# Optimization experiments

Measured on AMD Instinct MI355X. Metric: run time of the kernel, lower is better.

## Reference

```python
import jax, jax.numpy as jnp
import numpy as np

B, T, C, L = 256, 256, 1024, 64
NEG = jnp.float32(-1e30)  # finite stand-in for -inf (safe under exp)
EPS = 1e-7  # keras.backend.epsilon()


def setup_inputs() -> dict:
    key = jax.random.key(0)
    k1, k2 = jax.random.split(key)
    # y_pred: softmax-like probabilities (Keras ctc_batch_cost expects probs)
    y_pred = jax.random.uniform(k1, (B, T, C), dtype=jnp.float32)
    y_true = jax.random.randint(k2, (B, L), 0, C - 1, dtype=jnp.int64)  # blank = C-1 excluded
    return {"y_true": y_true, "y_pred": y_pred}


def reference(y_true, y_pred):
    # Faithful to keras.backend.ctc_batch_cost with input_length=T, label_length=L:
    # logits = log(y_pred + eps); tf.nn.ctc_loss applies log_softmax internally; blank = C-1.
    b, t, c = y_pred.shape
    l = y_true.shape[1]
    blank = c - 1
    logp = jax.nn.log_softmax(jnp.log(y_pred + EPS), axis=-1)  # [B,T,C]

    # Extended label sequence: blank, l1, blank, l2, ..., blank  (length S = 2L+1)
    s = 2 * l + 1
    ext = jnp.full((b, s), blank, dtype=y_true.dtype).at[:, 1::2].set(y_true)  # [B,S]
    pos = jnp.arange(s)
    prev2 = jnp.concatenate([jnp.full((b, 2), blank, dtype=ext.dtype), ext[:, :-2]], axis=1)
    # transition s-2 -> s allowed only for non-blank labels differing from label two back
    skip_ok = (ext != blank) & (ext != prev2) & (pos >= 2)  # [B,S]

    # Emission log-probs gathered at extended labels: [B,T,S]
    emit = jnp.take_along_axis(logp, jnp.broadcast_to(ext[:, None, :], (b, t, s)), axis=2)

    # Forward DP (log-space) over time via scan
    alpha0 = jnp.where(pos < 2, emit[:, 0, :], NEG)  # only states 0,1 reachable at t=0

    def step(alpha, emit_t):
        a1 = alpha
        a2 = jnp.concatenate([jnp.full((b, 1), NEG), alpha[:, :-1]], axis=1)
        a3 = jnp.where(skip_ok, jnp.concatenate([jnp.full((b, 2), NEG), alpha[:, :-2]], axis=1), NEG)
        m = jnp.maximum(a1, jnp.maximum(a2, a3))
        alpha_new = m + jnp.log(jnp.exp(a1 - m) + jnp.exp(a2 - m) + jnp.exp(a3 - m)) + emit_t
        return alpha_new, None

    alphaT, _ = jax.lax.scan(step, alpha0, jnp.swapaxes(emit, 0, 1)[1:])  # scan over T-1 steps

    tail = alphaT[:, s - 2:]  # valid end states: last label or final blank
    m = jnp.max(tail, axis=1)
    loglik = m + jnp.log(jnp.sum(jnp.exp(tail - m[:, None]), axis=1))
    return -loglik[:, None]  # [B,1], matches ctc_batch_cost output shape
```

## Files before the change

### kernel.cpp

```cpp
#include <hip/hip_runtime.h>
#include <hip/hip_bf16.h>


#define NEGF (-1e30f)

__device__ __forceinline__ float lse2(float a, float b) {
    float m = fmaxf(a, b);
    return m + log2f(exp2f(a - m) + exp2f(b - m));
}
__device__ __forceinline__ float lse3(float a, float b, float c) {
    float m = fmaxf(fmaxf(a, b), c);
    return m + log2f(exp2f(a - m) + exp2f(b - m) + exp2f(c - m));
}

__global__ void __launch_bounds__(1024) ctc_fused_kernel(
    const float* __restrict__ y, const int* __restrict__ lab,
    float* __restrict__ out)
{
    __shared__ float lpl_s[256][64];
    __shared__ float lpb_s[256];

    const int b    = blockIdx.x;
    const int wave = threadIdx.x >> 6;
    const int lane = threadIdx.x & 63;

    const int myLab = lab[(b << 6) + lane];

    for (int i = 0; i < 16; ++i) {
        const int t = (wave << 4) + i;
        const float* __restrict__ yr = y + ((size_t)(b * 256 + t) << 10);
        const float4* __restrict__ yr4 = (const float4*)yr;
        float4 v0 = yr4[lane];
        float4 v1 = yr4[lane + 64];
        float4 v2 = yr4[lane + 128];
        float4 v3 = yr4[lane + 192];
        float s = (v0.x + v0.y + v0.z + v0.w) + (v1.x + v1.y + v1.z + v1.w)
                + (v2.x + v2.y + v2.z + v2.w) + (v3.x + v3.y + v3.z + v3.w);
        #pragma unroll
        for (int off = 32; off; off >>= 1) s += __shfl_xor(s, off);
        const float norm = log2f(s + 1.024e-4f);
        const float yv = yr[myLab];
        lpl_s[t][lane] = log2f(yv + 1e-7f) - norm;
        if (lane == 0)
            lpb_s[t] = log2f(yr[1023] + 1e-7f) - norm;
    }
    __syncthreads();

    if (wave != 0) return;

    const int prevLab = __shfl_up(myLab, 1);
    const bool skip   = (lane >= 1) && (myLab != prevLab);

    float eb = lpb_s[0];
    float el = lpl_s[0][lane];
    float a0 = (lane == 0) ? eb : NEGF;
    float a1 = (lane == 0) ? el : NEGF;
    float a2 = NEGF;

    for (int t = 1; t < 256; ++t) {
        eb = lpb_s[t];
        el = lpl_s[t][lane];
        float p1 = __shfl_up(a1, 1);
        if (lane == 0) p1 = NEGF;
        float a1_63 = __shfl(a1, 63);
        float n0 = lse2(a0, p1) + eb;
        float n1 = lse3(a1, a0, skip ? p1 : NEGF) + el;
        float n2 = lse2(a2, a1_63) + eb;
        a0 = n0; a1 = n1; a2 = n2;
    }

    float t127 = __shfl(a1, 63);
    float ll = lse2(t127, a2);
    if (lane == 0)
        out[b] = -ll * 0.6931471805599453f;
}

extern "C" void kernel_launch(void* const* d_in, const int* in_sizes, int n_in,
                              void* d_out, int out_size, void* d_ws, size_t ws_size,
                              hipStream_t stream) {
    const int*   y_true = (const int*)d_in[0];
    const float* y_pred = (const float*)d_in[1];
    float* out = (float*)d_out;

    ctc_fused_kernel<<<256, 1024, 0, stream>>>(y_pred, y_true, out);
}
```

Measured before the change: 421.9 us.

## Split CTC into separate emission and alpha-recursion kernels with LDS direct loads

Splits the fused kernel into two launches. The first computes the normalized label and blank emission log-probs across 4096 small blocks for better occupancy, then writes them to a workspace. The second loads each batch's emissions into LDS with global_load_lds and runs the serial alpha recursion, prefetching the next timestep's emissions from LDS. This trades an extra launch and a global round trip of about 16 MB for much higher parallelism in the bandwidth-bound reduction phase.

```diff
diff --git a/kernel.cpp b/kernel.cpp
--- a/kernel.cpp
+++ b/kernel.cpp
@@ -3,6 +3,9 @@
 
 
 #define NEGF (-1e30f)
+
+typedef __attribute__((address_space(1))) const unsigned int GUI;
+typedef __attribute__((address_space(3))) unsigned int LUI;
 
 __device__ __forceinline__ float lse2(float a, float b) {
     float m = fmaxf(a, b);
@@ -13,22 +16,20 @@
     return m + log2f(exp2f(a - m) + exp2f(b - m) + exp2f(c - m));
 }
 
-__global__ void __launch_bounds__(1024) ctc_fused_kernel(
+__global__ void __launch_bounds__(256) emit_kernel(
     const float* __restrict__ y, const int* __restrict__ lab,
-    float* __restrict__ out)
+    float* __restrict__ lpl, float* __restrict__ lpb)
 {
-    __shared__ float lpl_s[256][64];
-    __shared__ float lpb_s[256];
-
-    const int b    = blockIdx.x;
     const int wave = threadIdx.x >> 6;
     const int lane = threadIdx.x & 63;
-
+    const int row0 = (blockIdx.x << 4) + (wave << 2);
+    const int b    = row0 >> 8;
     const int myLab = lab[(b << 6) + lane];
 
-    for (int i = 0; i < 16; ++i) {
-        const int t = (wave << 4) + i;
-        const float* __restrict__ yr = y + ((size_t)(b * 256 + t) << 10);
+    #pragma unroll
+    for (int r = 0; r < 4; ++r) {
+        const int row = row0 + r;
+        const float* __restrict__ yr = y + ((size_t)row << 10);
         const float4* __restrict__ yr4 = (const float4*)yr;
         float4 v0 = yr4[lane];
         float4 v1 = yr4[lane + 64];
@@ -38,33 +39,72 @@
                 + (v2.x + v2.y + v2.z + v2.w) + (v3.x + v3.y + v3.z + v3.w);
         #pragma unroll
         for (int off = 32; off; off >>= 1) s += __shfl_xor(s, off);
+
         const float norm = log2f(s + 1.024e-4f);
         const float yv = yr[myLab];
-        lpl_s[t][lane] = log2f(yv + 1e-7f) - norm;
+        const float nb = yr[1023];
+        lpl[((size_t)row << 6) + lane] = log2f(yv + 1e-7f) - norm;
         if (lane == 0)
-            lpb_s[t] = log2f(yr[1023] + 1e-7f) - norm;
+            lpb[row] = log2f(nb + 1e-7f) - norm;
     }
+}
+
+__global__ void __launch_bounds__(256) ctc_alpha_kernel(
+    const int* __restrict__ lab,
+    const float* __restrict__ lpl, const float* __restrict__ lpb,
+    float* __restrict__ out)
+{
+    __shared__ float lpl_s[256 * 64];
+    __shared__ float lpb_s[256];
+
+    const int b    = blockIdx.x;
+    const int wave = threadIdx.x >> 6;
+    const int lane = threadIdx.x & 63;
+
+    const float* __restrict__ gb = lpl + ((size_t)b << 14);
+    #pragma unroll
+    for (int c = 0; c < 16; ++c) {
+        const int off = (wave << 12) + (c << 8) + (lane << 2);
+        __builtin_amdgcn_global_load_lds((GUI*)(gb + off), (LUI*)(lpl_s + off),
+                                         16, 0, 0);
+    }
+    if (wave == 0) {
+        __builtin_amdgcn_global_load_lds((GUI*)(lpb + (b << 8) + lane),
+                                         (LUI*)(lpb_s + lane), 4, 0, 0);
+        __builtin_amdgcn_global_load_lds((GUI*)(lpb + (b << 8) + 64 + lane),
+                                         (LUI*)(lpb_s + 64 + lane), 4, 0, 0);
+        __builtin_amdgcn_global_load_lds((GUI*)(lpb + (b << 8) + 128 + lane),
+                                         (LUI*)(lpb_s + 128 + lane), 4, 0, 0);
+        __builtin_amdgcn_global_load_lds((GUI*)(lpb + (b << 8) + 192 + lane),
+                                         (LUI*)(lpb_s + 192 + lane), 4, 0, 0);
+    }
+    __builtin_amdgcn_s_waitcnt(0);
     __syncthreads();
 
     if (wave != 0) return;
 
+    const int myLab   = lab[(b << 6) + lane];
     const int prevLab = __shfl_up(myLab, 1);
     const bool skip   = (lane >= 1) && (myLab != prevLab);
 
     float eb = lpb_s[0];
-    float el = lpl_s[0][lane];
+    float el = lpl_s[lane];
     float a0 = (lane == 0) ? eb : NEGF;
     float a1 = (lane == 0) ? el : NEGF;
     float a2 = NEGF;
 
+    float ebp = lpb_s[1];
+    float elp = lpl_s[64 + lane];
+
     for (int t = 1; t < 256; ++t) {
-        eb = lpb_s[t];
-        el = lpl_s[t][lane];
+        eb = ebp; el = elp;
+        if (t < 255) { ebp = lpb_s[t + 1]; elp = lpl_s[((t + 1) << 6) + lane]; }
         float p1 = __shfl_up(a1, 1);
         if (lane == 0) p1 = NEGF;
+        float sp1 = skip ? p1 : NEGF;
         float a1_63 = __shfl(a1, 63);
         float n0 = lse2(a0, p1) + eb;
-        float n1 = lse3(a1, a0, skip ? p1 : NEGF) + el;
+        float n1 = lse3(a1, a0, sp1) + el;
         float n2 = lse2(a2, a1_63) + eb;
         a0 = n0; a1 = n1; a2 = n2;
     }
@@ -82,5 +122,9 @@
     const float* y_pred = (const float*)d_in[1];
     float* out = (float*)d_out;
 
-    ctc_fused_kernel<<<256, 1024, 0, stream>>>(y_pred, y_true, out);
+    float* lpl = (float*)d_ws;
+    float* lpb = lpl + (size_t)256 * 256 * 64;
+
+    emit_kernel<<<4096, 256, 0, stream>>>(y_pred, y_true, lpl, lpb);
+    ctc_alpha_kernel<<<256, 256, 0, stream>>>(y_true, lpl, lpb, out);
 }
```

New measurement: 413.4 us. 1.02x faster.
